# Optimization experiments

Hardware: AMD Instinct MI355X
Metric: run time of the kernel (lower is better)

## Reference

```python
import jax, jax.numpy as jnp
import numpy as np

BS, N, T, D, R = 64, 256, 32, 512, 8
DK = D // R  # 64 == key_feature_dim


def setup_inputs() -> dict:
    key = jax.random.key(0)
    ks = jax.random.split(key, 20)
    s = 0.02
    p = lambda k, shape: jax.random.normal(k, shape, jnp.float32) * s
    return {
        "v": jax.random.normal(ks[0], (BS, N, D), jnp.float32),
        "b": jax.random.normal(ks[1], (BS, N, D), jnp.float32),
        "v_mask": jnp.ones((BS, N), jnp.float32),
        "t": jax.random.normal(ks[2], (BS, T, D), jnp.float32),
        "t_mask": jnp.ones((BS, T), jnp.float32),
        "WG1_w": p(ks[3], (D, D)), "WG1_b": p(ks[4], (D,)),
        "WG2_w": p(ks[5], (D, D)), "WG2_b": p(ks[6], (D,)),
        "WK_w": p(ks[7], (D, D)), "WK_b": p(ks[8], (D,)),
        "WQ_w": p(ks[9], (D, D)), "WQ_b": p(ks[10], (D,)),
        "WV_w": p(ks[11], (D, D)), "WV_b": p(ks[12], (D,)),
        "tc_w": p(ks[13], (D, 1)), "tc_b": p(ks[14], (1,)),
        "tmap_w": p(ks[15], (D, N * N)), "tmap_b": p(ks[16], (N * N,)),
    }


def _forward(v, b, v_mask, t, t_mask,
             WG1_w, WG1_b, WG2_w, WG2_b, WK_w, WK_b, WQ_w, WQ_b, WV_w, WV_b,
             tc_w, tc_b, tmap_w, tmap_b):
    bs, num_obj, dim = v.shape
    n_rel = R
    dk = dim // n_rel  # dim_per_rel == dim_k

    def shape4(x):  # (bs, N, D) -> (bs, R, N, dk)
        return x.reshape(bs, num_obj, n_rel, dk).transpose(0, 2, 1, 3)

    # --- text summary branch ---
    t_m = t * t_mask[:, :, None]                       # (bs, T, D)
    tc = t_m @ tc_w + tc_b                             # (bs, T, 1)
    tc = jnp.where(t_mask[:, :, None] == 0, -jnp.inf, tc)
    t_sscore = jax.nn.sigmoid(tc)                      # sigmoid(-inf) = 0 for pad
    t_summary = jnp.einsum('btd,bt->bd', t_m, t_sscore[..., 0])   # (bs, D)
    tmap = jax.nn.relu(t_summary @ tmap_w + tmap_b)
    tmap = tmap.reshape(bs, 1, num_obj, num_obj)       # broadcast over relations

    # --- geometric pairwise score ---
    wg1 = shape4((b @ WG1_w + WG1_b) * v_mask[:, :, None])
    wg2 = shape4((b @ WG2_w + WG2_b) * v_mask[:, :, None])
    w_g = jax.nn.relu(jnp.einsum('brnd,brmd->brnm', wg1, wg2)) + tmap

    # --- scaled dot-product score ---
    wk = shape4(v @ WK_w + WK_b)
    wq = shape4(v @ WQ_w + WQ_b)
    scaled_dot = jnp.einsum('brnd,brmd->brnm', wk, wq) / jnp.sqrt(jnp.float32(dk))

    # --- combine, mask, softmax, weighted sum ---
    w_mn = jnp.log(jnp.maximum(w_g, 1e-6)) + scaled_dot
    w_mn = jnp.where((v_mask == 0)[:, None, None, :], -jnp.inf, w_mn)
    attn = jax.nn.softmax(w_mn, axis=-1)               # (bs, R, N, N)

    wv = shape4(v @ WV_w + WV_b)
    out = jnp.einsum('brnm,brmd->brnd', attn, wv)
    out = out.transpose(0, 2, 1, 3).reshape(bs, num_obj, dim)
    return out + v


def reference(v, b, v_mask, t, t_mask,
              WG1_w, WG1_b, WG2_w, WG2_b, WK_w, WK_b, WQ_w, WQ_b, WV_w, WV_b,
              tc_w, tc_b, tmap_w, tmap_b):
    return _forward(v, b, v_mask, t, t_mask,
                    WG1_w, WG1_b, WG2_w, WG2_b, WK_w, WK_b, WQ_w, WQ_b,
                    WV_w, WV_b, tc_w, tc_b, tmap_w, tmap_b)
```

## Files before the change

### kernel.cpp

```cpp
#include <hip/hip_runtime.h>
#include <math.h>

#define BS 64
#define NOBJ 256
#define TTOK 32
#define DIM 512
#define NREL 8
#define DKK 64
#define NN 65536

typedef __attribute__((ext_vector_type(8))) short bf16x8;
typedef __attribute__((ext_vector_type(4))) float f32x4;

__device__ __forceinline__ unsigned short f2bf(float x) {
    union { float f; unsigned int u; } c; c.f = x;
    unsigned int u = c.u;
    return (unsigned short)((u + 0x7fffu + ((u >> 16) & 1u)) >> 16);
}
__device__ __forceinline__ float bf2f(unsigned short h) {
    union { unsigned int u; float f; } c; c.u = ((unsigned int)h) << 16;
    return c.f;
}
__device__ __forceinline__ void gl2lds16(const unsigned short* g, unsigned short* l) {
    __builtin_amdgcn_global_load_lds((const __attribute__((address_space(1))) void*)g,
                                     (__attribute__((address_space(3))) void*)l, 16, 0, 0);
}

__global__ void k_text(const float* __restrict__ tt, const float* __restrict__ t_mask,
                       const float* __restrict__ tc_w, const float* __restrict__ tc_b,
                       unsigned short* __restrict__ ts_bf) {
    int b = blockIdx.x;
    int tid = threadIdx.x;
    __shared__ float red[TTOK][8];
    __shared__ float sc[TTOK];
    {
        int tok = tid >> 3, seg = tid & 7;
        const float* tp = tt + (size_t)(b * TTOK + tok) * DIM + seg * 64;
        const float* wp = tc_w + seg * 64;
        float s = 0.f;
#pragma unroll
        for (int i = 0; i < 16; ++i) {
            float4 a = *(const float4*)(tp + i * 4);
            float4 w = *(const float4*)(wp + i * 4);
            s += a.x * w.x + a.y * w.y + a.z * w.z + a.w * w.w;
        }
        red[tok][seg] = s;
    }
    __syncthreads();
    if (tid < TTOK) {
        float s = 0.f;
#pragma unroll
        for (int i = 0; i < 8; ++i) s += red[tid][i];
        float m = t_mask[b * TTOK + tid];
        float tc = m * s + tc_b[0];
        float sig = 1.f / (1.f + __expf(-tc));
        sc[tid] = (m != 0.f) ? m * sig : 0.f;
    }
    __syncthreads();
    for (int d = tid; d < DIM; d += 256) {
        float acc = 0.f;
#pragma unroll
        for (int tok = 0; tok < TTOK; ++tok)
            acc += tt[(size_t)(b * TTOK + tok) * DIM + d] * sc[tok];
        ts_bf[b * DIM + d] = f2bf(acc);
    }
}

__global__ void k_convert(const float* __restrict__ v, const float* __restrict__ b,
                          unsigned short* __restrict__ v_bf, unsigned short* __restrict__ b_bf) {
    const float* src = blockIdx.y ? b : v;
    unsigned short* dst = blockIdx.y ? b_bf : v_bf;
    size_t i = ((size_t)blockIdx.x * 256 + threadIdx.x) * 4;
    float4 a = *(const float4*)(src + i);
    ushort4 o;
    o.x = f2bf(a.x); o.y = f2bf(a.y); o.z = f2bf(a.z); o.w = f2bf(a.w);
    *(ushort4*)(dst + i) = o;
}

__global__ void k_wt(const float* __restrict__ w0, const float* __restrict__ w1,
                     const float* __restrict__ w2, const float* __restrict__ w3,
                     const float* __restrict__ w4, unsigned short* __restrict__ WT) {
    int wsel = blockIdx.z;
    const float* W = wsel == 0 ? w0 : wsel == 1 ? w1 : wsel == 2 ? w2 : wsel == 3 ? w3 : w4;
    int k0 = blockIdx.x * 64, d0 = blockIdx.y * 64;
    __shared__ float tile[64][65];
    int tid = threadIdx.x;
#pragma unroll
    for (int p = 0; p < 16; ++p) {
        int lin = p * 256 + tid;
        int kk = lin >> 6, dd = lin & 63;
        tile[kk][dd] = W[(size_t)(k0 + kk) * DIM + d0 + dd];
    }
    __syncthreads();
    unsigned short* outp = WT + (size_t)wsel * DIM * DIM;
#pragma unroll
    for (int p = 0; p < 16; ++p) {
        int lin = p * 256 + tid;
        int dd = lin >> 6, kk = lin & 63;
        outp[(size_t)(d0 + dd) * DIM + k0 + kk] = f2bf(tile[kk][dd]);
    }
}

__launch_bounds__(256)
__global__ void k_tmap(const unsigned short* __restrict__ ts_bf,
                       const float* __restrict__ tmap_w, const float* __restrict__ tmap_b,
                       unsigned short* __restrict__ tmap) {
    int j0 = blockIdx.x * 64;
    int tid = threadIdx.x;
    int w = tid >> 6, lane = tid & 63, q = lane >> 4, li = lane & 15;
    __shared__ __align__(16) unsigned short Bt[64][40];
    f32x4 acc[4];
#pragma unroll
    for (int ct = 0; ct < 4; ++ct) acc[ct] = (f32x4){0.f, 0.f, 0.f, 0.f};

    for (int ks = 0; ks < 16; ++ks) {
        int k0 = ks * 32;
#pragma unroll
        for (int p = 0; p < 8; ++p) {
            int kk = (tid >> 6) + p * 4;
            int c = tid & 63;
            Bt[c][kk] = f2bf(tmap_w[(size_t)(k0 + kk) * NN + j0 + c]);
        }
        __syncthreads();
        bf16x8 a = *(const bf16x8*)(ts_bf + (size_t)(w * 16 + li) * DIM + k0 + q * 8);
#pragma unroll
        for (int ct = 0; ct < 4; ++ct) {
            bf16x8 bb = *(const bf16x8*)(&Bt[ct * 16 + li][q * 8]);
            acc[ct] = __builtin_amdgcn_mfma_f32_16x16x32_bf16(a, bb, acc[ct], 0, 0, 0);
        }
        __syncthreads();
    }
#pragma unroll
    for (int ct = 0; ct < 4; ++ct) {
        int j = j0 + ct * 16 + li;
        float bias = tmap_b[j];
#pragma unroll
        for (int i = 0; i < 4; ++i) {
            int bb = w * 16 + q * 4 + i;
            float val = fmaxf(acc[ct][i] + bias, 0.f);
            tmap[(size_t)bb * NN + j] = f2bf(val);
        }
    }
}

__launch_bounds__(256)
__global__ void k_proj(const unsigned short* __restrict__ v_bf, const unsigned short* __restrict__ b_bf,
                       const unsigned short* __restrict__ WT,
                       const float* __restrict__ bias0, const float* __restrict__ bias1,
                       const float* __restrict__ bias2, const float* __restrict__ bias3,
                       const float* __restrict__ bias4, const float* __restrict__ v_mask,
                       unsigned short* __restrict__ wg1, unsigned short* __restrict__ wg2,
                       unsigned short* __restrict__ wk, unsigned short* __restrict__ wq,
                       unsigned short* __restrict__ wvT) {
    int bx = blockIdx.x;
    int by = blockIdx.y;
    int m0 = bx * 128;
    int wsel = by >> 2;
    const unsigned short* A = (wsel < 2) ? b_bf : v_bf;
    int tid = threadIdx.x;
    int w = tid >> 6, lane = tid & 63, q = lane >> 4, li = lane & 15;
    int rh = w & 1, ch = w >> 1;

    __shared__ __align__(16) unsigned short smem[128 * 136];
    unsigned short* As = smem;
    unsigned short* Bs = smem + 8192;

    f32x4 acc[4][4];
#pragma unroll
    for (int rt = 0; rt < 4; ++rt)
#pragma unroll
        for (int ct = 0; ct < 4; ++ct) acc[rt][ct] = (f32x4){0.f, 0.f, 0.f, 0.f};

    const unsigned short* WTb = WT + (size_t)by * 128 * DIM;

    int rl = lane >> 3;
    int lseg = (lane & 7) ^ rl;
    const unsigned short* Agp[4];
    const unsigned short* Bgp[4];
    unsigned short* Alp[4];
    unsigned short* Blp[4];
#pragma unroll
    for (int c4 = 0; c4 < 4; ++c4) {
        int c = w * 4 + c4;
        int row = c * 8 + rl;
        Agp[c4] = A + (size_t)(m0 + row) * DIM + lseg * 8;
        Bgp[c4] = WTb + (size_t)row * DIM + lseg * 8;
        Alp[c4] = As + c * 512;
        Blp[c4] = Bs + c * 512;
    }

    int arow = (rh * 64 + li) * 64;
    int brow = (ch * 64 + li) * 64;
    int sseg0 = ((q) ^ (li & 7)) * 8;
    int sseg1 = ((4 + q) ^ (li & 7)) * 8;

    for (int ks = 0; ks < 8; ++ks) {
        int k0 = ks * 64;
#pragma unroll
        for (int c4 = 0; c4 < 4; ++c4) {
            gl2lds16(Agp[c4] + k0, Alp[c4]);
            gl2lds16(Bgp[c4] + k0, Blp[c4]);
        }
        __syncthreads();
#pragma unroll
        for (int j = 0; j < 2; ++j) {
            int sseg = j ? sseg1 : sseg0;
            bf16x8 af[4], bfr[4];
#pragma unroll
            for (int rt = 0; rt < 4; ++rt)
                af[rt] = *(const bf16x8*)(As + arow + rt * 1024 + sseg);
#pragma unroll
            for (int ct = 0; ct < 4; ++ct)
                bfr[ct] = *(const bf16x8*)(Bs + brow + ct * 1024 + sseg);
#pragma unroll
            for (int rt = 0; rt < 4; ++rt)
#pragma unroll
                for (int ct = 0; ct < 4; ++ct)
                    acc[rt][ct] = __builtin_amdgcn_mfma_f32_16x16x32_bf16(af[rt], bfr[ct], acc[rt][ct], 0, 0, 0);
        }
        __syncthreads();
    }

    const float* bias = wsel == 0 ? bias0 : wsel == 1 ? bias1 : wsel == 2 ? bias2 : wsel == 3 ? bias3 : bias4;
    int dblk = (by & 3) * 128;

    unsigned short (*T)[136] = (unsigned short (*)[136])smem;
    if (wsel < 4) {
#pragma unroll
        for (int ct = 0; ct < 4; ++ct) {
            int d = dblk + ch * 64 + ct * 16 + li;
            float bs = bias[d];
#pragma unroll
            for (int rt = 0; rt < 4; ++rt) {
#pragma unroll
                for (int i = 0; i < 4; ++i) {
                    int nl = rh * 64 + rt * 16 + q * 4 + i;
                    float val = acc[rt][ct][i] + bs;
                    if (wsel < 2) val *= v_mask[m0 + nl];
                    T[nl][ch * 64 + ct * 16 + li] = f2bf(val);
                }
            }
        }
        __syncthreads();
        unsigned short* dstb = wsel == 0 ? wg1 : wsel == 1 ? wg2 : wsel == 2 ? wk : wq;
        int dc = lane & 15;
#pragma unroll
        for (int rr = 0; rr < 8; ++rr) {
            int outer = w * 32 + rr * 4 + (lane >> 4);
            *(bf16x8*)(dstb + (size_t)(m0 + outer) * DIM + dblk + dc * 8) =
                *(const bf16x8*)(&T[outer][dc * 8]);
        }
    } else {
#pragma unroll
        for (int ct = 0; ct < 4; ++ct) {
            int dl = ch * 64 + ct * 16 + li;
            float bs = bias[dblk + dl];
#pragma unroll
            for (int rt = 0; rt < 4; ++rt) {
#pragma unroll
                for (int i = 0; i < 4; ++i) {
                    int nl = rh * 64 + rt * 16 + q * 4 + i;
                    T[dl][nl] = f2bf(acc[rt][ct][i] + bs);
                }
            }
        }
        __syncthreads();
        int b = m0 >> 8, nbase = m0 & 255;
        int dc = lane & 15;
#pragma unroll
        for (int rr = 0; rr < 8; ++rr) {
            int outer = w * 32 + rr * 4 + (lane >> 4);
            int d = dblk + outer;
            int r = d >> 6, dk = d & 63;
            *(bf16x8*)(wvT + ((size_t)(b * NREL + r) * DKK + dk) * NOBJ + nbase + dc * 8) =
                *(const bf16x8*)(&T[outer][dc * 8]);
        }
    }
}

__launch_bounds__(256)
__global__ void k_attn(const unsigned short* __restrict__ wg1, const unsigned short* __restrict__ wg2,
                       const unsigned short* __restrict__ wk, const unsigned short* __restrict__ wq,
                       const unsigned short* __restrict__ wvT,
                       const unsigned short* __restrict__ tmap, const float* __restrict__ v_mask,
                       const float* __restrict__ v, float* __restrict__ out) {
    int L = blockIdx.x;
    int x = L & 7, jj = L >> 3;
    int b = x + 8 * (jj >> 4);
    int inner = jj & 15;
    int r = inner >> 1, half = inner & 1;
    int br = b * NREL + r;

    int tid = threadIdx.x;
    int w = tid >> 6, lane = tid & 63, q = lane >> 4, li = lane & 15;
    int n0 = half * 128 + w * 32;

    __shared__ __align__(16) unsigned short P_lds[4][2][32][36];

    bf16x8 ag[2][2], ak[2][2];
    {
        const unsigned short* g1b = wg1 + (size_t)(b * NOBJ + n0 + li) * DIM + r * DKK + q * 8;
        const unsigned short* kb  = wk  + (size_t)(b * NOBJ + n0 + li) * DIM + r * DKK + q * 8;
#pragma unroll
        for (int rt = 0; rt < 2; ++rt)
#pragma unroll
            for (int kt = 0; kt < 2; ++kt) {
                ag[rt][kt] = *(const bf16x8*)(g1b + (size_t)rt * 16 * DIM + kt * 32);
                ak[rt][kt] = *(const bf16x8*)(kb + (size_t)rt * 16 * DIM + kt * 32);
            }
    }

    f32x4 O[2][4];
    float lsum[2][4];
#pragma unroll
    for (int rt = 0; rt < 2; ++rt) {
#pragma unroll
        for (int dt = 0; dt < 4; ++dt) O[rt][dt] = (f32x4){0.f, 0.f, 0.f, 0.f};
#pragma unroll
        for (int i = 0; i < 4; ++i) lsum[rt][i] = 0.f;
    }

    const unsigned short* tb = tmap + ((size_t)b << 16) + (n0 + q * 4) * 256 + li;

    bf16x8 vbp[4];

    auto qk_softmax = [&](int j, int c0, int buf) {
        bf16x8 bg[2][2], bq[2][2];
        {
            const unsigned short* g2b = wg2 + (size_t)(b * NOBJ + c0 + li) * DIM + r * DKK + q * 8;
            const unsigned short* qb  = wq  + (size_t)(b * NOBJ + c0 + li) * DIM + r * DKK + q * 8;
#pragma unroll
            for (int ct = 0; ct < 2; ++ct)
#pragma unroll
                for (int kt = 0; kt < 2; ++kt) {
                    bg[ct][kt] = *(const bf16x8*)(g2b + (size_t)ct * 16 * DIM + kt * 32);
                    bq[ct][kt] = *(const bf16x8*)(qb + (size_t)ct * 16 * DIM + kt * 32);
                }
        }
        float vm0 = v_mask[b * NOBJ + c0 + li];
        float vm1 = v_mask[b * NOBJ + c0 + 16 + li];

#pragma unroll
        for (int rt = 0; rt < 2; ++rt) {
#pragma unroll
            for (int ct = 0; ct < 2; ++ct) {
                f32x4 aG = (f32x4){0.f, 0.f, 0.f, 0.f};
                f32x4 aK = (f32x4){0.f, 0.f, 0.f, 0.f};
#pragma unroll
                for (int kt = 0; kt < 2; ++kt) {
                    aG = __builtin_amdgcn_mfma_f32_16x16x32_bf16(ag[rt][kt], bg[ct][kt], aG, 0, 0, 0);
                    aK = __builtin_amdgcn_mfma_f32_16x16x32_bf16(ak[rt][kt], bq[ct][kt], aK, 0, 0, 0);
                }
                float vm = ct ? vm1 : vm0;
#pragma unroll
                for (int i = 0; i < 4; ++i) {
                    float tm = bf2f(tb[(rt * 16 + i) * 256 + c0 + ct * 16]);
                    float g = fmaxf(fmaxf(aG[i], 0.f) + tm, 1e-6f);
                    float p = (vm == 0.f) ? 0.f : g * __expf(aK[i] * 0.125f);
                    lsum[rt][i] += p;
                    P_lds[w][buf][rt * 16 + q * 4 + i][ct * 16 + li] = f2bf(p);
                }
            }
        }
    };
    auto load_vb = [&](int c0) {
#pragma unroll
        for (int dt = 0; dt < 4; ++dt)
            vbp[dt] = *(const bf16x8*)(wvT + (size_t)(br * DKK + dt * 16 + li) * NOBJ + c0 + q * 8);
    };
    auto pv = [&](int buf) {
        bf16x8 pa[2];
#pragma unroll
        for (int rt = 0; rt < 2; ++rt)
            pa[rt] = *(const bf16x8*)(&P_lds[w][buf][rt * 16 + li][q * 8]);
#pragma unroll
        for (int rt = 0; rt < 2; ++rt)
#pragma unroll
            for (int dt = 0; dt < 4; ++dt)
                O[rt][dt] = __builtin_amdgcn_mfma_f32_16x16x32_bf16(pa[rt], vbp[dt], O[rt][dt], 0, 0, 0);
    };

    qk_softmax(0, 0, 0);
    load_vb(0);

    for (int j = 1; j < 8; ++j) {
        int c0 = j * 32;
        pv((j - 1) & 1);
        qk_softmax(j, c0, j & 1);
        load_vb(c0);
    }
    pv(1);

#pragma unroll
    for (int rt = 0; rt < 2; ++rt) {
        float linv[4];
#pragma unroll
        for (int i = 0; i < 4; ++i) {
            float s = lsum[rt][i];
            s += __shfl_xor(s, 1);
            s += __shfl_xor(s, 2);
            s += __shfl_xor(s, 4);
            s += __shfl_xor(s, 8);
            linv[i] = 1.f / s;
        }
#pragma unroll
        for (int dt = 0; dt < 4; ++dt) {
#pragma unroll
            for (int i = 0; i < 4; ++i) {
                int n = n0 + rt * 16 + q * 4 + i;
                size_t idx = (size_t)(b * NOBJ + n) * DIM + r * DKK + dt * 16 + li;
                out[idx] = O[rt][dt][i] * linv[i] + v[idx];
            }
        }
    }
}

extern "C" void kernel_launch(void* const* d_in, const int* in_sizes, int n_in,
                              void* d_out, int out_size, void* d_ws, size_t ws_size,
                              hipStream_t stream) {
    const float* v      = (const float*)d_in[0];
    const float* b      = (const float*)d_in[1];
    const float* v_mask = (const float*)d_in[2];
    const float* t      = (const float*)d_in[3];
    const float* t_mask = (const float*)d_in[4];
    const float* WG1_w  = (const float*)d_in[5];
    const float* WG1_b  = (const float*)d_in[6];
    const float* WG2_w  = (const float*)d_in[7];
    const float* WG2_b  = (const float*)d_in[8];
    const float* WK_w   = (const float*)d_in[9];
    const float* WK_b   = (const float*)d_in[10];
    const float* WQ_w   = (const float*)d_in[11];
    const float* WQ_b   = (const float*)d_in[12];
    const float* WV_w   = (const float*)d_in[13];
    const float* WV_b   = (const float*)d_in[14];
    const float* tc_w   = (const float*)d_in[15];
    const float* tc_b   = (const float*)d_in[16];
    const float* tmap_w = (const float*)d_in[17];
    const float* tmap_b = (const float*)d_in[18];
    float* out = (float*)d_out;

    char* ws = (char*)d_ws;
    size_t off = 0;
    auto alloc = [&](size_t bytes) {
        void* p = ws + off;
        off += (bytes + 255) & ~(size_t)255;
        return p;
    };
    unsigned short* ts_bf = (unsigned short*)alloc((size_t)BS * DIM * 2);
    unsigned short* tmap  = (unsigned short*)alloc((size_t)BS * NN * 2);
    unsigned short* v_bf  = (unsigned short*)alloc((size_t)BS * NOBJ * DIM * 2);
    unsigned short* b_bf  = (unsigned short*)alloc((size_t)BS * NOBJ * DIM * 2);
    unsigned short* WT    = (unsigned short*)alloc((size_t)5 * DIM * DIM * 2);
    unsigned short* wg1   = (unsigned short*)alloc((size_t)BS * NOBJ * DIM * 2);
    unsigned short* wg2   = (unsigned short*)alloc((size_t)BS * NOBJ * DIM * 2);
    unsigned short* wk    = (unsigned short*)alloc((size_t)BS * NOBJ * DIM * 2);
    unsigned short* wq    = (unsigned short*)alloc((size_t)BS * NOBJ * DIM * 2);
    unsigned short* wvT   = (unsigned short*)alloc((size_t)BS * NOBJ * DIM * 2);

    k_text<<<dim3(BS), dim3(256), 0, stream>>>(t, t_mask, tc_w, tc_b, ts_bf);
    k_convert<<<dim3(8192, 2), dim3(256), 0, stream>>>(v, b, v_bf, b_bf);
    k_wt<<<dim3(8, 8, 5), dim3(256), 0, stream>>>(WG1_w, WG2_w, WK_w, WQ_w, WV_w, WT);
    k_tmap<<<dim3(1024), dim3(256), 0, stream>>>(ts_bf, tmap_w, tmap_b, tmap);
    k_proj<<<dim3(128, 20), dim3(256), 0, stream>>>(v_bf, b_bf, WT,
                                                    WG1_b, WG2_b, WK_b, WQ_b, WV_b, v_mask,
                                                    wg1, wg2, wk, wq, wvT);
    k_attn<<<dim3(1024), dim3(256), 0, stream>>>(wg1, wg2, wk, wq, wvT, tmap, v_mask, v, out);
}
```

Baseline: 439.5 us.

## Double-buffer tmap and projection GEMM loads to overlap with MFMA

In k_tmap, the 32-row slice of tmap_w is now read with float4 loads that are prefetched into registers one step ahead. It is packed as bf16 pairs into a double-buffered, XOR-swizzled LDS tile, which removes one barrier per k-step. In k_proj, the shared buffer doubles so the next K tile's global-to-LDS loads are issued before computing on the current tile. The aim is to hide global memory latency behind MFMA work. The cost is more LDS per block, which may lower occupancy, and extra register pressure from the prefetched values.

```diff
diff --git a/kernel.cpp b/kernel.cpp
--- a/kernel.cpp
+++ b/kernel.cpp
@@ -108,27 +108,45 @@
     int j0 = blockIdx.x * 64;
     int tid = threadIdx.x;
     int w = tid >> 6, lane = tid & 63, q = lane >> 4, li = lane & 15;
-    __shared__ __align__(16) unsigned short Bt[64][40];
+    __shared__ __align__(16) unsigned short Bt[2][64][40];
     f32x4 acc[4];
 #pragma unroll
     for (int ct = 0; ct < 4; ++ct) acc[ct] = (f32x4){0.f, 0.f, 0.f, 0.f};
 
+    int rp = tid >> 4, c4 = tid & 15;
+    const float* gsrc = tmap_w + (size_t)(2 * rp) * NN + j0 + c4 * 4;
+    float4 f0 = *(const float4*)(gsrc);
+    float4 f1 = *(const float4*)(gsrc + NN);
+
     for (int ks = 0; ks < 16; ++ks) {
+        int cur = ks & 1;
+        {
+            float lo[4] = {f0.x, f0.y, f0.z, f0.w};
+            float hi[4] = {f1.x, f1.y, f1.z, f1.w};
+#pragma unroll
+            for (int e = 0; e < 4; ++e) {
+                int col = c4 * 4 + e;
+                int x = (col >> 3) & 3;
+                int pos = (2 * rp) ^ (x * 8);
+                unsigned int pk = (unsigned int)f2bf(lo[e]) | ((unsigned int)f2bf(hi[e]) << 16);
+                *(unsigned int*)(&Bt[cur][col][pos]) = pk;
+            }
+        }
+        if (ks < 15) {
+            const float* g = gsrc + (size_t)(ks + 1) * 32 * NN;
+            f0 = *(const float4*)(g);
+            f1 = *(const float4*)(g + NN);
+        }
+        __syncthreads();
         int k0 = ks * 32;
-#pragma unroll
-        for (int p = 0; p < 8; ++p) {
-            int kk = (tid >> 6) + p * 4;
-            int c = tid & 63;
-            Bt[c][kk] = f2bf(tmap_w[(size_t)(k0 + kk) * NN + j0 + c]);
-        }
-        __syncthreads();
         bf16x8 a = *(const bf16x8*)(ts_bf + (size_t)(w * 16 + li) * DIM + k0 + q * 8);
 #pragma unroll
         for (int ct = 0; ct < 4; ++ct) {
-            bf16x8 bb = *(const bf16x8*)(&Bt[ct * 16 + li][q * 8]);
+            int col = ct * 16 + li;
+            int x = (col >> 3) & 3;
+            bf16x8 bb = *(const bf16x8*)(&Bt[cur][col][(q ^ x) * 8]);
             acc[ct] = __builtin_amdgcn_mfma_f32_16x16x32_bf16(a, bb, acc[ct], 0, 0, 0);
         }
-        __syncthreads();
     }
 #pragma unroll
     for (int ct = 0; ct < 4; ++ct) {
@@ -161,9 +179,7 @@
     int w = tid >> 6, lane = tid & 63, q = lane >> 4, li = lane & 15;
     int rh = w & 1, ch = w >> 1;
 
-    __shared__ __align__(16) unsigned short smem[128 * 136];
-    unsigned short* As = smem;
-    unsigned short* Bs = smem + 8192;
+    __shared__ __align__(16) unsigned short smem[32768];
 
     f32x4 acc[4][4];
 #pragma unroll
@@ -185,8 +201,8 @@
         int row = c * 8 + rl;
         Agp[c4] = A + (size_t)(m0 + row) * DIM + lseg * 8;
         Bgp[c4] = WTb + (size_t)row * DIM + lseg * 8;
-        Alp[c4] = As + c * 512;
-        Blp[c4] = Bs + c * 512;
+        Alp[c4] = smem + c * 512;
+        Blp[c4] = smem + 8192 + c * 512;
     }
 
     int arow = (rh * 64 + li) * 64;
@@ -194,24 +210,36 @@
     int sseg0 = ((q) ^ (li & 7)) * 8;
     int sseg1 = ((4 + q) ^ (li & 7)) * 8;
 
+#pragma unroll
+    for (int c4 = 0; c4 < 4; ++c4) {
+        gl2lds16(Agp[c4], Alp[c4]);
+        gl2lds16(Bgp[c4], Blp[c4]);
+    }
+    __syncthreads();
+
     for (int ks = 0; ks < 8; ++ks) {
-        int k0 = ks * 64;
-#pragma unroll
-        for (int c4 = 0; c4 < 4; ++c4) {
-            gl2lds16(Agp[c4] + k0, Alp[c4]);
-            gl2lds16(Bgp[c4] + k0, Blp[c4]);
-        }
-        __syncthreads();
+        int cur = ks & 1;
+        if (ks < 7) {
+            int k0 = (ks + 1) * 64;
+            int noff = (cur ^ 1) * 16384;
+#pragma unroll
+            for (int c4 = 0; c4 < 4; ++c4) {
+                gl2lds16(Agp[c4] + k0, Alp[c4] + noff);
+                gl2lds16(Bgp[c4] + k0, Blp[c4] + noff);
+            }
+        }
+        const unsigned short* Asb = smem + cur * 16384;
+        const unsigned short* Bsb = Asb + 8192;
 #pragma unroll
         for (int j = 0; j < 2; ++j) {
             int sseg = j ? sseg1 : sseg0;
             bf16x8 af[4], bfr[4];
 #pragma unroll
             for (int rt = 0; rt < 4; ++rt)
-                af[rt] = *(const bf16x8*)(As + arow + rt * 1024 + sseg);
+                af[rt] = *(const bf16x8*)(Asb + arow + rt * 1024 + sseg);
 #pragma unroll
             for (int ct = 0; ct < 4; ++ct)
-                bfr[ct] = *(const bf16x8*)(Bs + brow + ct * 1024 + sseg);
+                bfr[ct] = *(const bf16x8*)(Bsb + brow + ct * 1024 + sseg);
 #pragma unroll
             for (int rt = 0; rt < 4; ++rt)
 #pragma unroll
```

Measured after the change: 428.9 us. 2.4% less time.
